# Kernel optimization log

Measured on AMD Instinct MI355X. Metric: run time of the kernel, lower is better.

## Reference

```python
import jax, jax.numpy as jnp
import numpy as np

# Spike nonlinearity with straight-through surrogate gradient
# fwd: z = (v_scaled > 0); bwd: dz/dv = clamp(1 - |v_scaled|, min=0)
@jax.custom_vjp
def spike(v_scaled):
    return (v_scaled > 0).astype(v_scaled.dtype)

def _spike_fwd(v_scaled):
    return spike(v_scaled), v_scaled

def _spike_bwd(v_scaled, g):
    return (g * jnp.maximum(1.0 - jnp.abs(v_scaled), 0.0),)

spike.defvjp(_spike_fwd, _spike_bwd)

_H = np.array([-0.00285825, 0.09859432, 0.07954306, 0.08560576, 0.0910411, 0.10557652,
               0.04608637, 0.07096123, 0.01989892, 0.03412642, 0.03321506, 0.01300904,
               -0.02348068, 0.06102338, -0.00509757, 0.00051896], dtype=np.float32)
_D = np.array([0.04908372, -0.00948576, 0.00083943, 0.07961489, 0.08128168, 0.02395899,
               0.05197346, 0.01595683, 0.02185501, 0.01893722, 0.0074682, -0.00088913,
               0.01660369, 0.00298292, 0.0071363, 0.00279426], dtype=np.float32)
_T = np.array([0.20153396, -0.01304637, -0.19541621, 0.19903184, 0.1529713, -0.00479887,
               0.07102165, 0.02109929, 0.01368383, -0.00360851, -0.01454873, -0.03991705,
               -0.00440092, -0.06122432, -0.02989412, -0.04975629], dtype=np.float32)


def setup_inputs() -> dict:
    key = jax.random.key(0)
    x = jax.random.normal(key, (64, 1024, 1024), dtype=jnp.float32)
    return {
        "x": x,
        "h": jnp.asarray(_H),
        "d": jnp.asarray(_D),
        "T": jnp.asarray(_T),
    }


def reference(x, h, d, T):
    signs = jax.lax.stop_gradient(jnp.sign(x))  # detached in original
    x_abs = jnp.abs(x)

    def step(carry, hdT):
        v, z, out = carry
        ht, dt, Tt = hdT
        v = v - z * ht
        v_scaled = (v - Tt) / (jnp.abs(v) + 1.0)
        z = spike(v_scaled)
        out = out + z * dt
        return (v, z, out), None

    init = (x_abs, jnp.zeros_like(x_abs), jnp.zeros_like(x_abs))
    (_, _, out), _ = jax.lax.scan(step, init, (h, d, T))  # K=16 steps
    return out * signs
```

## Files before the change

### kernel.cpp

```cpp
#include <hip/hip_runtime.h>


#define BIN_B0 0x3D800000u
#define BIN_B1 0x3FC00000u
#define BIN_RANGE 0x02400000u
#define NBIN 4096
#define CMAX 12
#define BP_CAP 2048

#define W_CNT 0
#define W_FLAG 1
#define W_LO 2
#define W_HI 3
#define W_LUT 4
#define W_BP (W_LUT + NBIN)
#define WS_WORDS (W_BP + BP_CAP)

__device__ __forceinline__ int predmask16(float a, const float* __restrict__ hh,
                                          const float* __restrict__ TT) {
    float v = a, z = 0.0f;
    int m = 0;
#pragma unroll
    for (int k = 0; k < 16; ++k) {
        v = fmaf(-z, hh[k], v);
        int zb = (v > TT[k]) ? 1 : 0;
        z = zb ? 1.0f : 0.0f;
        m |= zb << k;
    }
    return m;
}

__device__ __forceinline__ unsigned int valbits(int m, const float* __restrict__ dd) {
    float acc = 0.0f;
#pragma unroll
    for (int k = 0; k < 16; ++k)
        acc = ((m >> k) & 1) ? (acc + dd[k]) : acc;
    return __float_as_uint(acc);
}

__device__ __forceinline__ float scan_exact(unsigned int ab, const float* __restrict__ hh,
                                            const float* __restrict__ dd,
                                            const float* __restrict__ TT) {
    float v = __uint_as_float(ab), z = 0.0f, acc = 0.0f;
#pragma unroll
    for (int k = 0; k < 16; ++k) {
        v = fmaf(-z, hh[k], v);
        z = (v > TT[k]) ? 1.0f : 0.0f;
        acc = fmaf(z, dd[k], acc);
    }
    return acc;
}

__global__ void snn_init(unsigned int* __restrict__ ws) {
    if (threadIdx.x == 0) { ws[W_CNT] = 0u; ws[W_FLAG] = 0u; }
}

__global__ __launch_bounds__(256) void snn_build(
    const float* __restrict__ h, const float* __restrict__ d,
    const float* __restrict__ T, unsigned int* __restrict__ ws) {
    const int u = blockIdx.x * 256 + threadIdx.x;
    if (u >= NBIN + 2) return;
    float hh[16], dd[16], TT[16];
#pragma unroll
    for (int k = 0; k < 16; ++k) { hh[k] = h[k]; dd[k] = d[k]; TT[k] = T[k]; }

    if (u == NBIN) {
        int mA = predmask16(__uint_as_float(0u), hh, TT);
        int mB = predmask16(__uint_as_float(BIN_B0 - 1u), hh, TT);
        if (mA == mB) ws[W_LO] = valbits(mA, dd);
        else { ws[W_LO] = 0u; atomicOr(&ws[W_FLAG], 1u); }
        return;
    }
    if (u == NBIN + 1) {
        int mA = predmask16(__uint_as_float(BIN_B1), hh, TT);
        int mB = predmask16(__uint_as_float(0x7F7FFFFFu), hh, TT);
        if (mA == mB) ws[W_HI] = valbits(mA, dd);
        else { ws[W_HI] = 0u; atomicOr(&ws[W_FLAG], 1u); }
        return;
    }

    const unsigned int Lb = BIN_B0 + (unsigned int)u * 9216u;
    const unsigned int Hb = Lb + 9215u;
    const int mL = predmask16(__uint_as_float(Lb), hh, TT);
    const int mH = predmask16(__uint_as_float(Hb), hh, TT);
    if (mL == mH) { ws[W_LUT + u] = valbits(mL, dd); return; }

    unsigned int bp[CMAX];
    int vm[CMAX + 1];
    vm[0] = mL;
    int cnt = 0, cur = mL;
    unsigned int anchor = Lb;
    bool bad = false;
    while (cur != mH) {
        if (cnt == CMAX) { bad = true; break; }
        unsigned int lo = anchor, hi = Hb;
        int mhi = mH;
        while (hi - lo > 1u) {
            unsigned int mid = lo + ((hi - lo) >> 1);
            int mm = predmask16(__uint_as_float(mid), hh, TT);
            if (mm == cur) lo = mid; else { hi = mid; mhi = mm; }
        }
        bp[cnt] = hi;
        vm[cnt + 1] = mhi;
        ++cnt;
        cur = mhi;
        anchor = hi;
    }
    if (bad) { atomicOr(&ws[W_FLAG], 1u); ws[W_LUT + u] = 0u; return; }

    const unsigned int need = 2u * (unsigned int)cnt + 1u;
    const unsigned int start = atomicAdd(&ws[W_CNT], need);
    if (start + need > BP_CAP) { atomicOr(&ws[W_FLAG], 1u); ws[W_LUT + u] = 0u; return; }
    for (int k = 0; k < cnt; ++k) ws[W_BP + start + k] = bp[k];
    for (int j = 0; j <= cnt; ++j)
        ws[W_BP + start + cnt + j] = valbits(vm[j], dd);
    ws[W_LUT + u] = 0x7F800000u | ((unsigned int)cnt << 19) | start;
}

__device__ __forceinline__ float lut_elem(float xe,
                                          const unsigned int* __restrict__ lutS,
                                          const unsigned int* __restrict__ bpS,
                                          unsigned int lo_e, unsigned int hi_e) {
    const unsigned int u = __float_as_uint(xe);
    const unsigned int sb = u & 0x80000000u;
    const unsigned int ab = u & 0x7FFFFFFFu;
    unsigned int t = ab - BIN_B0;
    t = (t > BIN_RANGE - 1u) ? (BIN_RANGE - 1u) : t;
    const unsigned int bin = ((t >> 10) * 58255u) >> 19;
    unsigned int eb = lutS[bin];
    eb = (ab < BIN_B0) ? lo_e : eb;
    eb = (ab >= BIN_B1) ? hi_e : eb;
    if ((eb & 0x7F800000u) == 0x7F800000u) {
        const unsigned int s = eb & 0x7FFFFu;
        const unsigned int c = (eb >> 19) & 0xFu;
        unsigned int j = 0;
        for (unsigned int k = 0; k < c; ++k)
            j += (ab >= bpS[s + k]) ? 1u : 0u;
        eb = bpS[s + c + j];
    }
    const float r = __uint_as_float(eb ^ sb);
    return (xe == 0.0f) ? 0.0f : r;
}

__global__ __launch_bounds__(256) void snn_apply(
    const float* __restrict__ x, const float* __restrict__ h,
    const float* __restrict__ d, const float* __restrict__ T,
    float* __restrict__ out, const unsigned int* __restrict__ ws,
    int n8, int n4, int n) {
    __shared__ unsigned int lutS[NBIN];
    __shared__ unsigned int bpS[BP_CAP];
    const int tid = threadIdx.x;

    for (int i = tid; i < NBIN; i += 256) lutS[i] = ws[W_LUT + i];
    for (int i = tid; i < BP_CAP; i += 256) bpS[i] = ws[W_BP + i];
    const unsigned int flag = ws[W_FLAG];
    const unsigned int lo_e = ws[W_LO];
    const unsigned int hi_e = ws[W_HI];
    __syncthreads();

    const float4* __restrict__ x4 = reinterpret_cast<const float4*>(x);
    float4* __restrict__ o4 = reinterpret_cast<float4*>(out);
    const int gtid = blockIdx.x * blockDim.x + tid;
    const int nt = gridDim.x * blockDim.x;

    if (flag == 0u) {
#define APPLY4(vv)                                                             \
        {                                                                      \
            float4 ov;                                                         \
            ov.x = lut_elem(vv.x, lutS, bpS, lo_e, hi_e);                      \
            ov.y = lut_elem(vv.y, lutS, bpS, lo_e, hi_e);                      \
            ov.z = lut_elem(vv.z, lutS, bpS, lo_e, hi_e);                      \
            ov.w = lut_elem(vv.w, lutS, bpS, lo_e, hi_e);                      \
            vv = ov;                                                           \
        }
        int i = gtid;
        if (i < n8) {
            float4 ca = x4[2 * i], cb = x4[2 * i + 1];
            int nx = i + nt;
            while (nx < n8) {
                float4 pa = x4[2 * nx], pb = x4[2 * nx + 1];
                APPLY4(ca); APPLY4(cb);
                o4[2 * i] = ca; o4[2 * i + 1] = cb;
                ca = pa; cb = pb;
                i = nx; nx += nt;
            }
            APPLY4(ca); APPLY4(cb);
            o4[2 * i] = ca; o4[2 * i + 1] = cb;
        }
        for (int j = n8 * 2 + gtid; j < n4; j += nt) {
            float4 v = x4[j];
            APPLY4(v);
            o4[j] = v;
        }
        for (int j = n4 * 4 + gtid; j < n; j += nt)
            out[j] = lut_elem(x[j], lutS, bpS, lo_e, hi_e);
#undef APPLY4
    } else {
        float hh[16], dd[16], TT[16];
#pragma unroll
        for (int k = 0; k < 16; ++k) { hh[k] = h[k]; dd[k] = d[k]; TT[k] = T[k]; }
        for (int j = gtid; j < n4; j += nt) {
            float4 v = x4[j], ov;
            float* pi = &v.x;
            float* po = &ov.x;
#pragma unroll
            for (int e = 0; e < 4; ++e) {
                float xe = pi[e];
                float acc = scan_exact(__float_as_uint(xe) & 0x7FFFFFFFu, hh, dd, TT);
                unsigned int rb =
                    __float_as_uint(acc) ^ (__float_as_uint(xe) & 0x80000000u);
                po[e] = (xe == 0.0f) ? 0.0f : __uint_as_float(rb);
            }
            o4[j] = ov;
        }
        for (int j = n4 * 4 + gtid; j < n; j += nt) {
            float xe = x[j];
            float acc = scan_exact(__float_as_uint(xe) & 0x7FFFFFFFu, hh, dd, TT);
            unsigned int rb = __float_as_uint(acc) ^ (__float_as_uint(xe) & 0x80000000u);
            out[j] = (xe == 0.0f) ? 0.0f : __uint_as_float(rb);
        }
    }
}

__global__ __launch_bounds__(256) void snn_direct(
    const float* __restrict__ x, const float* __restrict__ h,
    const float* __restrict__ d, const float* __restrict__ T,
    float* __restrict__ out, int n4, int n) {
    float hh[16], dd[16], TT[16];
#pragma unroll
    for (int k = 0; k < 16; ++k) { hh[k] = h[k]; dd[k] = d[k]; TT[k] = T[k]; }
    const float4* __restrict__ x4 = reinterpret_cast<const float4*>(x);
    float4* __restrict__ o4 = reinterpret_cast<float4*>(out);
    const int gtid = blockIdx.x * blockDim.x + threadIdx.x;
    const int nt = gridDim.x * blockDim.x;
    for (int i = gtid; i < n4; i += nt) {
        float4 v = x4[i], ov;
        float* pi = &v.x;
        float* po = &ov.x;
#pragma unroll
        for (int e = 0; e < 4; ++e) {
            float xe = pi[e];
            float acc = scan_exact(__float_as_uint(xe) & 0x7FFFFFFFu, hh, dd, TT);
            unsigned int rb =
                __float_as_uint(acc) ^ (__float_as_uint(xe) & 0x80000000u);
            po[e] = (xe == 0.0f) ? 0.0f : __uint_as_float(rb);
        }
        o4[i] = ov;
    }
    for (int j = n4 * 4 + gtid; j < n; j += nt) {
        float xe = x[j];
        float acc = scan_exact(__float_as_uint(xe) & 0x7FFFFFFFu, hh, dd, TT);
        unsigned int rb = __float_as_uint(acc) ^ (__float_as_uint(xe) & 0x80000000u);
        out[j] = (xe == 0.0f) ? 0.0f : __uint_as_float(rb);
    }
}

extern "C" void kernel_launch(void* const* d_in, const int* in_sizes, int n_in,
                              void* d_out, int out_size, void* d_ws, size_t ws_size,
                              hipStream_t stream) {
    const float* x = (const float*)d_in[0];
    const float* h = (const float*)d_in[1];
    const float* d = (const float*)d_in[2];
    const float* T = (const float*)d_in[3];
    float* out = (float*)d_out;

    const int n = in_sizes[0];
    const int n4 = n / 4;
    const int n8 = n / 8;

    if (ws_size < (size_t)WS_WORDS * 4) {
        int grid = 2048;
        const int needed = (n4 + 255) / 256;
        if (grid > needed) grid = needed > 0 ? needed : 1;
        snn_direct<<<grid, 256, 0, stream>>>(x, h, d, T, out, n4, n);
        return;
    }

    unsigned int* ws = (unsigned int*)d_ws;
    snn_init<<<1, 64, 0, stream>>>(ws);
    snn_build<<<(NBIN + 2 + 255) / 256, 256, 0, stream>>>(h, d, T, ws);

    int grid = 1536;
    const int needed = (n8 + 255) / 256;
    if (grid > needed) grid = needed > 0 ? needed : 1;
    snn_apply<<<grid, 256, 0, stream>>>(x, h, d, T, out, ws, n8, n4, n);
}
```

Measured before the change: 143.7 us.

## Parallelize breakpoint search across a wavefront and use nontemporal output stores

Measured after the change: 208.7 us. 1.45x slower.

```diff
diff --git a/kernel.cpp b/kernel.cpp
--- a/kernel.cpp
+++ b/kernel.cpp
@@ -5,8 +5,10 @@
 #define BIN_B1 0x3FC00000u
 #define BIN_RANGE 0x02400000u
 #define NBIN 4096
-#define CMAX 12
+#define GAP 144u
+#define CMAX 15
 #define BP_CAP 2048
+#define MIXEDTAG 0xFFFFFFFFu
 
 #define W_CNT 0
 #define W_FLAG 1
@@ -16,6 +18,8 @@
 #define W_BP (W_LUT + NBIN)
 #define WS_WORDS (W_BP + BP_CAP)
 
+typedef float f32x4v __attribute__((ext_vector_type(4)));
+
 __device__ __forceinline__ int predmask16(float a, const float* __restrict__ hh,
                                           const float* __restrict__ TT) {
     float v = a, z = 0.0f;
@@ -51,70 +55,127 @@
     return acc;
 }
 
-__global__ void snn_init(unsigned int* __restrict__ ws) {
-    if (threadIdx.x == 0) { ws[W_CNT] = 0u; ws[W_FLAG] = 0u; }
-}
-
-__global__ __launch_bounds__(256) void snn_build(
+__global__ __launch_bounds__(256) void snn_classify(
     const float* __restrict__ h, const float* __restrict__ d,
     const float* __restrict__ T, unsigned int* __restrict__ ws) {
     const int u = blockIdx.x * 256 + threadIdx.x;
-    if (u >= NBIN + 2) return;
     float hh[16], dd[16], TT[16];
 #pragma unroll
     for (int k = 0; k < 16; ++k) { hh[k] = h[k]; dd[k] = d[k]; TT[k] = T[k]; }
 
-    if (u == NBIN) {
+    if (u == 0) {
+        ws[W_CNT] = 0u;
+        unsigned int flag = 0u;
         int mA = predmask16(__uint_as_float(0u), hh, TT);
         int mB = predmask16(__uint_as_float(BIN_B0 - 1u), hh, TT);
-        if (mA == mB) ws[W_LO] = valbits(mA, dd);
-        else { ws[W_LO] = 0u; atomicOr(&ws[W_FLAG], 1u); }
-        return;
-    }
-    if (u == NBIN + 1) {
-        int mA = predmask16(__uint_as_float(BIN_B1), hh, TT);
-        int mB = predmask16(__uint_as_float(0x7F7FFFFFu), hh, TT);
-        if (mA == mB) ws[W_HI] = valbits(mA, dd);
-        else { ws[W_HI] = 0u; atomicOr(&ws[W_FLAG], 1u); }
-        return;
-    }
+        if (mA == mB) ws[W_LO] = valbits(mA, dd); else { ws[W_LO] = 0u; flag = 1u; }
+        mA = predmask16(__uint_as_float(BIN_B1), hh, TT);
+        mB = predmask16(__uint_as_float(0x7F7FFFFFu), hh, TT);
+        if (mA == mB) ws[W_HI] = valbits(mA, dd); else { ws[W_HI] = 0u; flag = 1u; }
+        ws[W_FLAG] = flag;
+    }
+    if (u >= NBIN) return;
 
     const unsigned int Lb = BIN_B0 + (unsigned int)u * 9216u;
-    const unsigned int Hb = Lb + 9215u;
     const int mL = predmask16(__uint_as_float(Lb), hh, TT);
-    const int mH = predmask16(__uint_as_float(Hb), hh, TT);
-    if (mL == mH) { ws[W_LUT + u] = valbits(mL, dd); return; }
-
-    unsigned int bp[CMAX];
-    int vm[CMAX + 1];
-    vm[0] = mL;
-    int cnt = 0, cur = mL;
-    unsigned int anchor = Lb;
-    bool bad = false;
-    while (cur != mH) {
-        if (cnt == CMAX) { bad = true; break; }
-        unsigned int lo = anchor, hi = Hb;
-        int mhi = mH;
-        while (hi - lo > 1u) {
-            unsigned int mid = lo + ((hi - lo) >> 1);
-            int mm = predmask16(__uint_as_float(mid), hh, TT);
-            if (mm == cur) lo = mid; else { hi = mid; mhi = mm; }
-        }
-        bp[cnt] = hi;
-        vm[cnt + 1] = mhi;
-        ++cnt;
-        cur = mhi;
-        anchor = hi;
-    }
-    if (bad) { atomicOr(&ws[W_FLAG], 1u); ws[W_LUT + u] = 0u; return; }
-
-    const unsigned int need = 2u * (unsigned int)cnt + 1u;
-    const unsigned int start = atomicAdd(&ws[W_CNT], need);
-    if (start + need > BP_CAP) { atomicOr(&ws[W_FLAG], 1u); ws[W_LUT + u] = 0u; return; }
-    for (int k = 0; k < cnt; ++k) ws[W_BP + start + k] = bp[k];
-    for (int j = 0; j <= cnt; ++j)
-        ws[W_BP + start + cnt + j] = valbits(vm[j], dd);
-    ws[W_LUT + u] = 0x7F800000u | ((unsigned int)cnt << 19) | start;
+    const int mH = predmask16(__uint_as_float(Lb + 9215u), hh, TT);
+    ws[W_LUT + u] = (mL == mH) ? valbits(mL, dd) : MIXEDTAG;
+}
+
+__global__ __launch_bounds__(64) void snn_refine(
+    const float* __restrict__ h, const float* __restrict__ d,
+    const float* __restrict__ T, unsigned int* __restrict__ ws) {
+    const unsigned int b = blockIdx.x;
+    if (ws[W_LUT + b] != MIXEDTAG) return;
+
+    __shared__ unsigned int posS[CMAX + 1];
+    __shared__ int mskS[CMAX + 1];
+    __shared__ int cntS;
+    const int l = threadIdx.x;
+    if (l == 0) cntS = 0;
+    __syncthreads();
+
+    float hh[16], dd[16], TT[16];
+#pragma unroll
+    for (int k = 0; k < 16; ++k) { hh[k] = h[k]; dd[k] = d[k]; TT[k] = T[k]; }
+
+    const unsigned int Lb = BIN_B0 + b * 9216u;
+    const int mL = predmask16(__uint_as_float(Lb), hh, TT);
+    unsigned int po = (unsigned int)(l + 1) * GAP;
+    po = (po > 9215u) ? 9215u : po;
+    const int ml = predmask16(__uint_as_float(Lb + po), hh, TT);
+    int mprev = __shfl_up(ml, 1);
+    if (l == 0) mprev = mL;
+    const bool mixed = (mprev != ml);
+    unsigned long long bal = __ballot(mixed);
+
+    while (bal) {
+        const int g = __ffsll((long long)bal) - 1;
+        bal &= bal - 1ull;
+        const unsigned int gstart = Lb + (unsigned int)g * GAP;
+        unsigned int gend = (unsigned int)(g + 1) * GAP;
+        gend = (gend > 9215u) ? 9215u : gend;
+        const unsigned int width = (Lb + gend) - gstart;
+        const int m_glo = __shfl(mprev, g);
+        int mk0 = predmask16(__uint_as_float(gstart + 1u + (unsigned int)l), hh, TT);
+        int mk1 = predmask16(__uint_as_float(gstart + 65u + (unsigned int)l), hh, TT);
+        int mk2 = predmask16(__uint_as_float(gstart + 129u + (unsigned int)l), hh, TT);
+        int pm0 = __shfl_up(mk0, 1);
+        int pm1 = __shfl_up(mk1, 1);
+        int pm2 = __shfl_up(mk2, 1);
+        const int w0 = __shfl(mk0, 63);
+        const int w1 = __shfl(mk1, 63);
+        if (l == 0) { pm0 = m_glo; pm1 = w0; pm2 = w1; }
+        if ((unsigned int)l < width && pm0 != mk0) {
+            int s = atomicAdd(&cntS, 1);
+            if (s <= CMAX) { posS[s] = gstart + 1u + l; mskS[s] = mk0; }
+        }
+        if ((unsigned int)(l + 64) < width && pm1 != mk1) {
+            int s = atomicAdd(&cntS, 1);
+            if (s <= CMAX) { posS[s] = gstart + 65u + l; mskS[s] = mk1; }
+        }
+        if ((unsigned int)(l + 128) < width && pm2 != mk2) {
+            int s = atomicAdd(&cntS, 1);
+            if (s <= CMAX) { posS[s] = gstart + 129u + l; mskS[s] = mk2; }
+        }
+        __syncthreads();
+    }
+    __syncthreads();
+
+    if (l == 0) {
+        int c = cntS;
+        if (c < 1 || c > CMAX) {
+            atomicOr(&ws[W_FLAG], 1u);
+            ws[W_LUT + b] = 0u;
+        } else {
+            for (int i = 1; i < c; ++i) {
+                unsigned int p = posS[i];
+                int m = mskS[i];
+                int j = i - 1;
+                while (j >= 0 && posS[j] > p) {
+                    posS[j + 1] = posS[j];
+                    mskS[j + 1] = mskS[j];
+                    --j;
+                }
+                posS[j + 1] = p;
+                mskS[j + 1] = m;
+            }
+            const unsigned int need = 2u * (unsigned int)c + 1u;
+            const unsigned int start = atomicAdd(&ws[W_CNT], need);
+            if (start + need > BP_CAP) {
+                atomicOr(&ws[W_FLAG], 1u);
+                ws[W_LUT + b] = 0u;
+            } else {
+                const int mLb = predmask16(__uint_as_float(Lb), hh, TT);
+                for (int k = 0; k < c; ++k) ws[W_BP + start + k] = posS[k];
+                ws[W_BP + start + c] = valbits(mLb, dd);
+                for (int j = 0; j < c; ++j)
+                    ws[W_BP + start + c + 1 + j] = valbits(mskS[j], dd);
+                ws[W_LUT + b] =
+                    0x7F800000u | ((unsigned int)c << 19) | start;
+            }
+        }
+    }
 }
 
 __device__ __forceinline__ float lut_elem(float xe,
@@ -164,14 +225,14 @@
     const int nt = gridDim.x * blockDim.x;
 
     if (flag == 0u) {
-#define APPLY4(vv)                                                             \
+#define APPLY4NT(vv, dst)                                                      \
         {                                                                      \
-            float4 ov;                                                         \
+            f32x4v ov;                                                         \
             ov.x = lut_elem(vv.x, lutS, bpS, lo_e, hi_e);                      \
             ov.y = lut_elem(vv.y, lutS, bpS, lo_e, hi_e);                      \
             ov.z = lut_elem(vv.z, lutS, bpS, lo_e, hi_e);                      \
             ov.w = lut_elem(vv.w, lutS, bpS, lo_e, hi_e);                      \
-            vv = ov;                                                           \
+            __builtin_nontemporal_store(ov, reinterpret_cast<f32x4v*>(dst));   \
         }
         int i = gtid;
         if (i < n8) {
@@ -179,22 +240,21 @@
             int nx = i + nt;
             while (nx < n8) {
                 float4 pa = x4[2 * nx], pb = x4[2 * nx + 1];
-                APPLY4(ca); APPLY4(cb);
-                o4[2 * i] = ca; o4[2 * i + 1] = cb;
+                APPLY4NT(ca, o4 + 2 * i);
+                APPLY4NT(cb, o4 + 2 * i + 1);
                 ca = pa; cb = pb;
                 i = nx; nx += nt;
             }
-            APPLY4(ca); APPLY4(cb);
-            o4[2 * i] = ca; o4[2 * i + 1] = cb;
+            APPLY4NT(ca, o4 + 2 * i);
+            APPLY4NT(cb, o4 + 2 * i + 1);
         }
         for (int j = n8 * 2 + gtid; j < n4; j += nt) {
             float4 v = x4[j];
-            APPLY4(v);
-            o4[j] = v;
+            APPLY4NT(v, o4 + j);
         }
         for (int j = n4 * 4 + gtid; j < n; j += nt)
             out[j] = lut_elem(x[j], lutS, bpS, lo_e, hi_e);
-#undef APPLY4
+#undef APPLY4NT
     } else {
         float hh[16], dd[16], TT[16];
 #pragma unroll
@@ -277,8 +337,8 @@
     }
 
     unsigned int* ws = (unsigned int*)d_ws;
-    snn_init<<<1, 64, 0, stream>>>(ws);
-    snn_build<<<(NBIN + 2 + 255) / 256, 256, 0, stream>>>(h, d, T, ws);
+    snn_classify<<<NBIN / 256, 256, 0, stream>>>(h, d, T, ws);
+    snn_refine<<<NBIN, 64, 0, stream>>>(h, d, T, ws);
 
     int grid = 1536;
     const int needed = (n8 + 255) / 256;
```
